# Performance work log

Hardware: AMD Instinct MI355X
Metric: run time of the kernel (lower is better)

Reference implementation:

```python
import jax, jax.numpy as jnp
import numpy as np

D_MODEL = 1024
NUM_HEADS = 16
DEPTH = D_MODEL // NUM_HEADS


def setup_inputs() -> dict:
    key = jax.random.key(0)
    ks = jax.random.split(key, 9)
    B, S = 4, 2048
    scale = 1.0 / np.sqrt(D_MODEL)
    x = jax.random.normal(ks[0], (B, S, D_MODEL), dtype=jnp.float32)
    wq = jax.random.uniform(ks[1], (D_MODEL, D_MODEL), jnp.float32, -scale, scale)
    bq = jax.random.uniform(ks[2], (D_MODEL,), jnp.float32, -scale, scale)
    wk = jax.random.uniform(ks[3], (D_MODEL, D_MODEL), jnp.float32, -scale, scale)
    bk = jax.random.uniform(ks[4], (D_MODEL,), jnp.float32, -scale, scale)
    wv = jax.random.uniform(ks[5], (D_MODEL, D_MODEL), jnp.float32, -scale, scale)
    bv = jax.random.uniform(ks[6], (D_MODEL,), jnp.float32, -scale, scale)
    wo = jax.random.uniform(ks[7], (D_MODEL, D_MODEL), jnp.float32, -scale, scale)
    bo = jax.random.uniform(ks[8], (D_MODEL,), jnp.float32, -scale, scale)
    return {"x": x, "wq": wq, "bq": bq, "wk": wk, "bk": bk,
            "wv": wv, "bv": bv, "wo": wo, "bo": bo}


def reference(x, wq, bq, wk, bk, wv, bv, wo, bo):
    B, S, _ = x.shape
    def heads(t):  # [B,S,D] -> [B,H,S,depth]
        return t.reshape(B, S, NUM_HEADS, DEPTH).transpose(0, 2, 1, 3)
    q = heads(x @ wq + bq)
    k = heads(x @ wk + bk)
    v = heads(x @ wv + bv)
    scores = jnp.einsum('bhqd,bhkd->bhqk', q, k) / jnp.sqrt(jnp.float32(DEPTH))
    attn = jax.nn.softmax(scores, axis=-1)
    out = jnp.einsum('bhqk,bhkd->bhqd', attn, v)
    out = out.transpose(0, 2, 1, 3).reshape(B, S, D_MODEL)
    return out @ wo + bo
```

## Files before the change

kernel.cpp:

```cpp
#include <hip/hip_runtime.h>
#include <cstdint>


typedef __bf16 bf16x8 __attribute__((ext_vector_type(8)));
typedef float f32x4 __attribute__((ext_vector_type(4)));
typedef int i32x4 __attribute__((ext_vector_type(4)));

#define CEXP 0.18033688011112042f

__device__ __forceinline__ unsigned short f2bf(float f) {
  union { float f; unsigned int u; } v; v.f = f;
  unsigned int r = v.u + 0x7FFFu + ((v.u >> 16) & 1u);
  return (unsigned short)(r >> 16);
}
__device__ __forceinline__ unsigned int fbits(float f) {
  union { float f; unsigned int u; } v; v.f = f; return v.u;
}

__device__ __forceinline__ void gl_lds16(const void* g, void* l) {
  __builtin_amdgcn_global_load_lds(
      (const __attribute__((address_space(1))) void*)(unsigned long long)g,
      (__attribute__((address_space(3))) void*)(unsigned int)(unsigned long long)l,
      16, 0, 0);
}

__global__ __launch_bounds__(256) void pack_x_kernel(const float* __restrict__ x,
                                                     unsigned short* __restrict__ xb) {
  int i = (blockIdx.x * 256 + threadIdx.x) * 4;
  float4 v = *(const float4*)(x + i);
  unsigned int lo = (unsigned int)f2bf(v.x) | ((unsigned int)f2bf(v.y) << 16);
  unsigned int hi = (unsigned int)f2bf(v.z) | ((unsigned int)f2bf(v.w) << 16);
  uint2 st; st.x = lo; st.y = hi;
  *(uint2*)(xb + i) = st;
}

__global__ __launch_bounds__(256) void pack_w_kernel(const float* __restrict__ wq,
                                                     const float* __restrict__ wk,
                                                     const float* __restrict__ wv,
                                                     const float* __restrict__ wo,
                                                     unsigned short* __restrict__ wqkvt,
                                                     unsigned short* __restrict__ wot) {
  __shared__ unsigned short T[64 * 66];
  int mat = blockIdx.x >> 8;
  int tile = blockIdx.x & 255;
  int tk = tile >> 4, tn = tile & 15;
  const float* W = (mat == 0) ? wq : (mat == 1) ? wk : (mat == 2) ? wv : wo;
  int t = threadIdx.x;
#pragma unroll
  for (int p = 0; p < 16; ++p) {
    int e = p * 256 + t;
    int r = e >> 6, c = e & 63;
    T[c * 66 + r] = f2bf(W[(tk * 64 + r) * 1024 + tn * 64 + c]);
  }
  __syncthreads();
  unsigned short* dst = (mat < 3) ? (wqkvt + mat * 1024 * 1024) : wot;
#pragma unroll
  for (int p = 0; p < 16; ++p) {
    int e = p * 256 + t;
    int nn = e >> 6, kk = e & 63;
    dst[(tn * 64 + nn) * 1024 + tk * 64 + kk] = T[nn * 66 + kk];
  }
}

template <int MODE>
__global__ __launch_bounds__(256) void gemm_bt_kernel(
    const unsigned short* __restrict__ A, const unsigned short* __restrict__ Bt,
    const float* __restrict__ b0, const float* __restrict__ b1, const float* __restrict__ b2,
    unsigned short* __restrict__ Qg, unsigned short* __restrict__ Kg,
    unsigned short* __restrict__ Vtg, float* __restrict__ Of) {
  __shared__ __align__(16) unsigned short As[128 * 64];
  __shared__ __align__(16) unsigned short Bs[128 * 64];
  const int t = threadIdx.x;
  const int lane = t & 63, wave = t >> 6;
  const int l15 = lane & 15, quad = lane >> 4;
  const int wm = wave & 1, wn = wave >> 1;
  const int m0 = blockIdx.x * 128, n0 = blockIdx.y * 128;

  f32x4 acc[4][4];
#pragma unroll
  for (int i = 0; i < 4; ++i)
#pragma unroll
    for (int j = 0; j < 4; ++j) acc[i][j] = (f32x4){0.f, 0.f, 0.f, 0.f};

  const int Xo0 = ((quad ^ (l15 & 7)) * 8);
  const int Xo1 = (((4 + quad) ^ (l15 & 7)) * 8);

  for (int k0 = 0; k0 < 1024; k0 += 64) {
    __syncthreads();
#pragma unroll
    for (int p = 0; p < 4; ++p) {
      int s = p * 256 + t;
      int row = s >> 3;
      int cc = (s & 7) ^ (row & 7);
      gl_lds16(A + (m0 + row) * 1024 + k0 + cc * 8, (void*)(As + (p * 256 + wave * 64) * 8));
      gl_lds16(Bt + (n0 + row) * 1024 + k0 + cc * 8, (void*)(Bs + (p * 256 + wave * 64) * 8));
    }
    __syncthreads();
#pragma unroll
    for (int kc = 0; kc < 2; ++kc) {
      const int Xo = kc ? Xo1 : Xo0;
      bf16x8 af[4], bfr[4];
#pragma unroll
      for (int mi = 0; mi < 4; ++mi)
        af[mi] = *(const bf16x8*)&As[(wm * 64 + mi * 16 + l15) * 64 + Xo];
#pragma unroll
      for (int ni = 0; ni < 4; ++ni)
        bfr[ni] = *(const bf16x8*)&Bs[(wn * 64 + ni * 16 + l15) * 64 + Xo];
#pragma unroll
      for (int mi = 0; mi < 4; ++mi)
#pragma unroll
        for (int ni = 0; ni < 4; ++ni)
          acc[mi][ni] = __builtin_amdgcn_mfma_f32_16x16x32_bf16(af[mi], bfr[ni], acc[mi][ni], 0, 0, 0);
    }
  }

  if (MODE == 0) {
    const int seg = blockIdx.y >> 3;
    const float* bias = (seg == 0) ? b0 : (seg == 1) ? b1 : b2;
    unsigned short* qk = (seg == 0) ? Qg : Kg;
#pragma unroll
    for (int mi = 0; mi < 4; ++mi)
#pragma unroll
      for (int ni = 0; ni < 4; ++ni) {
        int n = n0 + wn * 64 + ni * 16 + l15;
        int nn = n & 1023;
        float bb = bias[nn];
        int h = nn >> 6, d = nn & 63;
#pragma unroll
        for (int r = 0; r < 4; ++r) {
          int m = m0 + wm * 64 + mi * 16 + quad * 4 + r;
          int b = m >> 11, s = m & 2047;
          float val = acc[mi][ni][r] + bb;
          if (seg == 2) {
            int sp = (s & ~63) | (s & 32) | ((s & 12) << 1) | ((s & 16) >> 2) | (s & 3);
            Vtg[((b * 16 + h) * 64 + d) * 2048 + sp] = f2bf(val);
          } else {
            if (seg == 0) val *= CEXP;
            qk[((b * 16 + h) * 2048 + s) * 64 + d] = f2bf(val);
          }
        }
      }
  } else {
#pragma unroll
    for (int mi = 0; mi < 4; ++mi)
#pragma unroll
      for (int ni = 0; ni < 4; ++ni) {
        int n = n0 + wn * 64 + ni * 16 + l15;
        float bb = b0[n];
#pragma unroll
        for (int r = 0; r < 4; ++r) {
          int m = m0 + wm * 64 + mi * 16 + quad * 4 + r;
          Of[m * 1024 + n] = acc[mi][ni][r] + bb;
        }
      }
  }
}

__global__ __launch_bounds__(256) void attn_kernel(const unsigned short* __restrict__ Qg,
                                                   const unsigned short* __restrict__ Kg,
                                                   const unsigned short* __restrict__ Vtg,
                                                   unsigned short* __restrict__ Og) {
  __shared__ __align__(16) unsigned short smem[16384];
  const int t = threadIdx.x;
  const int lane = t & 63, wave = t >> 6;
  const int l15 = lane & 15, quad = lane >> 4;
  const int bid = blockIdx.x;
  const int bh = (bid & 7) * 8 + (bid >> 7);
  const int qt = (bid >> 3) & 15;

  const unsigned short* Qh = Qg + (bh * 2048 + qt * 128) * 64;
  const unsigned short* Kh = Kg + bh * 2048 * 64;
  const unsigned short* Vth = Vtg + bh * 64 * 2048;

#pragma unroll
  for (int p = 0; p < 4; ++p) {
    int s = p * 256 + t;
    int row = s >> 3, cc = (s & 7) ^ (row & 7);
    gl_lds16(Qh + row * 64 + cc * 8, (void*)(smem + (p * 256 + wave * 64) * 8));
  }
  __syncthreads();

  const int Xo0 = ((quad ^ (l15 & 7)) * 8);
  const int Xo1 = (((4 + quad) ^ (l15 & 7)) * 8);

  bf16x8 qf[2][2];
#pragma unroll
  for (int qi = 0; qi < 2; ++qi) {
    qf[qi][0] = *(const bf16x8*)&smem[(wave * 32 + qi * 16 + l15) * 64 + Xo0];
    qf[qi][1] = *(const bf16x8*)&smem[(wave * 32 + qi * 16 + l15) * 64 + Xo1];
  }

#pragma unroll
  for (int p = 0; p < 2; ++p) {
    int s = p * 256 + t;
    int row = s >> 3, cc = (s & 7) ^ (row & 7);
    gl_lds16(Kh + row * 64 + cc * 8, (void*)(smem + 8192 + (p * 256 + wave * 64) * 8));
    gl_lds16(Vth + row * 2048 + cc * 8, (void*)(smem + 12288 + (p * 256 + wave * 64) * 8));
  }

  f32x4 oacc[4][2];
#pragma unroll
  for (int di = 0; di < 4; ++di)
#pragma unroll
    for (int qi = 0; qi < 2; ++qi) oacc[di][qi] = (f32x4){0.f, 0.f, 0.f, 0.f};
  float lsum[2] = {0.f, 0.f};

  for (int kt = 0; kt < 32; ++kt) {
    __syncthreads();
    if (kt + 1 < 32) {
      const unsigned short* Kn = Kh + (kt + 1) * 64 * 64;
      const unsigned short* Vn = Vth + (kt + 1) * 64;
      unsigned short* Kd = smem + (((kt + 1) & 1) ? 0 : 8192);
      unsigned short* Vd = smem + (((kt + 1) & 1) ? 4096 : 12288);
#pragma unroll
      for (int p = 0; p < 2; ++p) {
        int s = p * 256 + t;
        int row = s >> 3, cc = (s & 7) ^ (row & 7);
        gl_lds16(Kn + row * 64 + cc * 8, (void*)(Kd + (p * 256 + wave * 64) * 8));
        gl_lds16(Vn + row * 2048 + cc * 8, (void*)(Vd + (p * 256 + wave * 64) * 8));
      }
    }
    const unsigned short* Ks = smem + ((kt & 1) ? 0 : 8192);
    const unsigned short* Vs = smem + ((kt & 1) ? 4096 : 12288);

    f32x4 sacc[4][2];
#pragma unroll
    for (int ki = 0; ki < 4; ++ki)
#pragma unroll
      for (int qi = 0; qi < 2; ++qi) sacc[ki][qi] = (f32x4){0.f, 0.f, 0.f, 0.f};
#pragma unroll
    for (int kc = 0; kc < 2; ++kc) {
      const int Xo = kc ? Xo1 : Xo0;
      bf16x8 kf[4];
#pragma unroll
      for (int ki = 0; ki < 4; ++ki)
        kf[ki] = *(const bf16x8*)&Ks[(ki * 16 + l15) * 64 + Xo];
#pragma unroll
      for (int ki = 0; ki < 4; ++ki)
#pragma unroll
        for (int qi = 0; qi < 2; ++qi)
          sacc[ki][qi] = __builtin_amdgcn_mfma_f32_16x16x32_bf16(kf[ki], qf[qi][kc], sacc[ki][qi], 0, 0, 0);
    }

    i32x4 pk[2][2];
#pragma unroll
    for (int qi = 0; qi < 2; ++qi) {
      float ls = 0.f;
#pragma unroll
      for (int kc = 0; kc < 2; ++kc)
#pragma unroll
        for (int u = 0; u < 2; ++u) {
          int ki = kc * 2 + u;
          float p0 = __builtin_amdgcn_exp2f(sacc[ki][qi][0]);
          float p1 = __builtin_amdgcn_exp2f(sacc[ki][qi][1]);
          float p2 = __builtin_amdgcn_exp2f(sacc[ki][qi][2]);
          float p3 = __builtin_amdgcn_exp2f(sacc[ki][qi][3]);
          ls += (p0 + p1) + (p2 + p3);
          pk[qi][kc][u * 2 + 0] =
              (int)__builtin_amdgcn_perm(fbits(p1) + 0x8000u, fbits(p0) + 0x8000u, 0x07060302u);
          pk[qi][kc][u * 2 + 1] =
              (int)__builtin_amdgcn_perm(fbits(p3) + 0x8000u, fbits(p2) + 0x8000u, 0x07060302u);
        }
      lsum[qi] += ls;
    }

#pragma unroll
    for (int kc = 0; kc < 2; ++kc) {
      const int Xo = kc ? Xo1 : Xo0;
      bf16x8 vf[4];
#pragma unroll
      for (int di = 0; di < 4; ++di)
        vf[di] = *(const bf16x8*)&Vs[(di * 16 + l15) * 64 + Xo];
#pragma unroll
      for (int di = 0; di < 4; ++di)
#pragma unroll
        for (int qi = 0; qi < 2; ++qi)
          oacc[di][qi] = __builtin_amdgcn_mfma_f32_16x16x32_bf16(
              vf[di], __builtin_bit_cast(bf16x8, pk[qi][kc]), oacc[di][qi], 0, 0, 0);
    }
  }

  const int b = bh >> 4, h = bh & 15;
#pragma unroll
  for (int qi = 0; qi < 2; ++qi) {
    float l = lsum[qi];
    l += __shfl_xor(l, 16);
    l += __shfl_xor(l, 32);
    float inv = 1.f / l;
    int q = qt * 128 + wave * 32 + qi * 16 + l15;
#pragma unroll
    for (int di = 0; di < 4; ++di) {
      unsigned int lo = (unsigned int)f2bf(oacc[di][qi][0] * inv) |
                        ((unsigned int)f2bf(oacc[di][qi][1] * inv) << 16);
      unsigned int hi = (unsigned int)f2bf(oacc[di][qi][2] * inv) |
                        ((unsigned int)f2bf(oacc[di][qi][3] * inv) << 16);
      uint2 st; st.x = lo; st.y = hi;
      *(uint2*)(Og + ((size_t)(b * 2048 + q) * 1024) + h * 64 + di * 16 + quad * 4) = st;
    }
  }
}

extern "C" void kernel_launch(void* const* d_in, const int* in_sizes, int n_in,
                              void* d_out, int out_size, void* d_ws, size_t ws_size,
                              hipStream_t stream) {
  const float* x  = (const float*)d_in[0];
  const float* wq = (const float*)d_in[1];
  const float* bq = (const float*)d_in[2];
  const float* wk = (const float*)d_in[3];
  const float* bk = (const float*)d_in[4];
  const float* wv = (const float*)d_in[5];
  const float* bv = (const float*)d_in[6];
  const float* wo = (const float*)d_in[7];
  const float* bo = (const float*)d_in[8];
  char* ws = (char*)d_ws;
  unsigned short* Xb    = (unsigned short*)(ws);
  unsigned short* Wqkvt = (unsigned short*)(ws + (16ull << 20));
  unsigned short* Wot   = (unsigned short*)(ws + (22ull << 20));
  unsigned short* Qg    = (unsigned short*)(ws + (24ull << 20));
  unsigned short* Kg    = (unsigned short*)(ws + (40ull << 20));
  unsigned short* Vtg   = (unsigned short*)(ws + (56ull << 20));
  unsigned short* Og    = (unsigned short*)(ws + (72ull << 20));

  pack_x_kernel<<<8192, 256, 0, stream>>>(x, Xb);
  pack_w_kernel<<<1024, 256, 0, stream>>>(wq, wk, wv, wo, Wqkvt, Wot);
  gemm_bt_kernel<0><<<dim3(64, 24), 256, 0, stream>>>(Xb, Wqkvt, bq, bk, bv,
                                                      Qg, Kg, Vtg, nullptr);
  attn_kernel<<<1024, 256, 0, stream>>>(Qg, Kg, Vtg, Og);
  gemm_bt_kernel<1><<<dim3(64, 8), 256, 0, stream>>>(Og, Wot, bo, nullptr, nullptr,
                                                     nullptr, nullptr, nullptr,
                                                     (float*)d_out);
}
```

Measured before the change: 292.7 us.

## Double-buffer GEMM LDS staging and merge bf16 pack kernels into one launch

The GEMM kernel now uses two LDS buffers. It prefetches the next K-tile with global_load_lds while MFMAs run on the current one, and it drops one barrier per iteration. This is meant to hide global load latency that was previously exposed between the staging and compute phases. The x and weight packing kernels are also fused into a single launch to save one launch gap. The cost is that LDS per block doubles to 64KB, which can lower occupancy, and the compiler may insert conservative waits that limit the overlap.

New measurement: 283.5 us. -3.2%, faster.

```diff
diff --git a/kernel.cpp b/kernel.cpp
--- a/kernel.cpp
+++ b/kernel.cpp
@@ -24,25 +24,28 @@
       16, 0, 0);
 }
 
-__global__ __launch_bounds__(256) void pack_x_kernel(const float* __restrict__ x,
-                                                     unsigned short* __restrict__ xb) {
-  int i = (blockIdx.x * 256 + threadIdx.x) * 4;
-  float4 v = *(const float4*)(x + i);
-  unsigned int lo = (unsigned int)f2bf(v.x) | ((unsigned int)f2bf(v.y) << 16);
-  unsigned int hi = (unsigned int)f2bf(v.z) | ((unsigned int)f2bf(v.w) << 16);
-  uint2 st; st.x = lo; st.y = hi;
-  *(uint2*)(xb + i) = st;
-}
-
-__global__ __launch_bounds__(256) void pack_w_kernel(const float* __restrict__ wq,
-                                                     const float* __restrict__ wk,
-                                                     const float* __restrict__ wv,
-                                                     const float* __restrict__ wo,
-                                                     unsigned short* __restrict__ wqkvt,
-                                                     unsigned short* __restrict__ wot) {
+__global__ __launch_bounds__(256) void pack_all_kernel(const float* __restrict__ x,
+                                                       const float* __restrict__ wq,
+                                                       const float* __restrict__ wk,
+                                                       const float* __restrict__ wv,
+                                                       const float* __restrict__ wo,
+                                                       unsigned short* __restrict__ xb,
+                                                       unsigned short* __restrict__ wqkvt,
+                                                       unsigned short* __restrict__ wot) {
+  int bid = blockIdx.x;
+  if (bid < 8192) {
+    int i = (bid * 256 + threadIdx.x) * 4;
+    float4 v = *(const float4*)(x + i);
+    unsigned int lo = (unsigned int)f2bf(v.x) | ((unsigned int)f2bf(v.y) << 16);
+    unsigned int hi = (unsigned int)f2bf(v.z) | ((unsigned int)f2bf(v.w) << 16);
+    uint2 st; st.x = lo; st.y = hi;
+    *(uint2*)(xb + i) = st;
+    return;
+  }
   __shared__ unsigned short T[64 * 66];
-  int mat = blockIdx.x >> 8;
-  int tile = blockIdx.x & 255;
+  bid -= 8192;
+  int mat = bid >> 8;
+  int tile = bid & 255;
   int tk = tile >> 4, tn = tile & 15;
   const float* W = (mat == 0) ? wq : (mat == 1) ? wk : (mat == 2) ? wv : wo;
   int t = threadIdx.x;
@@ -59,6 +62,20 @@
     int e = p * 256 + t;
     int nn = e >> 6, kk = e & 63;
     dst[(tn * 64 + nn) * 1024 + tk * 64 + kk] = T[nn * 66 + kk];
+  }
+}
+
+__device__ __forceinline__ void stage_tile(const unsigned short* __restrict__ Ag,
+                                           const unsigned short* __restrict__ Bg,
+                                           unsigned short* As, unsigned short* Bs,
+                                           int t, int wave) {
+#pragma unroll
+  for (int p = 0; p < 4; ++p) {
+    int s = p * 256 + t;
+    int row = s >> 3;
+    int cc = (s & 7) ^ (row & 7);
+    gl_lds16(Ag + row * 1024 + cc * 8, (void*)(As + (p * 256 + wave * 64) * 8));
+    gl_lds16(Bg + row * 1024 + cc * 8, (void*)(Bs + (p * 256 + wave * 64) * 8));
   }
 }
 
@@ -68,13 +85,14 @@
     const float* __restrict__ b0, const float* __restrict__ b1, const float* __restrict__ b2,
     unsigned short* __restrict__ Qg, unsigned short* __restrict__ Kg,
     unsigned short* __restrict__ Vtg, float* __restrict__ Of) {
-  __shared__ __align__(16) unsigned short As[128 * 64];
-  __shared__ __align__(16) unsigned short Bs[128 * 64];
+  __shared__ __align__(16) unsigned short S[32768];
   const int t = threadIdx.x;
   const int lane = t & 63, wave = t >> 6;
   const int l15 = lane & 15, quad = lane >> 4;
   const int wm = wave & 1, wn = wave >> 1;
   const int m0 = blockIdx.x * 128, n0 = blockIdx.y * 128;
+  const unsigned short* Ab = A + (size_t)m0 * 1024;
+  const unsigned short* Bb = Bt + (size_t)n0 * 1024;
 
   f32x4 acc[4][4];
 #pragma unroll
@@ -85,27 +103,26 @@
   const int Xo0 = ((quad ^ (l15 & 7)) * 8);
   const int Xo1 = (((4 + quad) ^ (l15 & 7)) * 8);
 
+  stage_tile(Ab, Bb, S, S + 8192, t, wave);
+
   for (int k0 = 0; k0 < 1024; k0 += 64) {
+    const int buf = (k0 >> 6) & 1;
+    unsigned short* Sc = S + buf * 16384;
     __syncthreads();
-#pragma unroll
-    for (int p = 0; p < 4; ++p) {
-      int s = p * 256 + t;
-      int row = s >> 3;
-      int cc = (s & 7) ^ (row & 7);
-      gl_lds16(A + (m0 + row) * 1024 + k0 + cc * 8, (void*)(As + (p * 256 + wave * 64) * 8));
-      gl_lds16(Bt + (n0 + row) * 1024 + k0 + cc * 8, (void*)(Bs + (p * 256 + wave * 64) * 8));
-    }
-    __syncthreads();
+    if (k0 < 1024 - 64) {
+      unsigned short* Sn = S + (buf ^ 1) * 16384;
+      stage_tile(Ab + k0 + 64, Bb + k0 + 64, Sn, Sn + 8192, t, wave);
+    }
 #pragma unroll
     for (int kc = 0; kc < 2; ++kc) {
       const int Xo = kc ? Xo1 : Xo0;
       bf16x8 af[4], bfr[4];
 #pragma unroll
       for (int mi = 0; mi < 4; ++mi)
-        af[mi] = *(const bf16x8*)&As[(wm * 64 + mi * 16 + l15) * 64 + Xo];
+        af[mi] = *(const bf16x8*)&Sc[(wm * 64 + mi * 16 + l15) * 64 + Xo];
 #pragma unroll
       for (int ni = 0; ni < 4; ++ni)
-        bfr[ni] = *(const bf16x8*)&Bs[(wn * 64 + ni * 16 + l15) * 64 + Xo];
+        bfr[ni] = *(const bf16x8*)&Sc[8192 + (wn * 64 + ni * 16 + l15) * 64 + Xo];
 #pragma unroll
       for (int mi = 0; mi < 4; ++mi)
 #pragma unroll
@@ -321,8 +338,7 @@
   unsigned short* Vtg   = (unsigned short*)(ws + (56ull << 20));
   unsigned short* Og    = (unsigned short*)(ws + (72ull << 20));
 
-  pack_x_kernel<<<8192, 256, 0, stream>>>(x, Xb);
-  pack_w_kernel<<<1024, 256, 0, stream>>>(wq, wk, wv, wo, Wqkvt, Wot);
+  pack_all_kernel<<<9216, 256, 0, stream>>>(x, wq, wk, wv, wo, Xb, Wqkvt, Wot);
   gemm_bt_kernel<0><<<dim3(64, 24), 256, 0, stream>>>(Xb, Wqkvt, bq, bk, bv,
                                                       Qg, Kg, Vtg, nullptr);
   attn_kernel<<<1024, 256, 0, stream>>>(Qg, Kg, Vtg, Og);
```
